# Performance work log

Hardware: AMD Instinct MI355X
Metric: run time of the kernel (lower is better)

## Reference

```python
import jax, jax.numpy as jnp
import numpy as np

B, T, E = 4, 2048, 1024
H = 16
HS = E // H  # head_size = d_model // num_heads, d_model == E here
D_FF = 4 * E
EPS = 1e-5


def _layernorm(x, g, b):
    mu = jnp.mean(x, axis=-1, keepdims=True)
    var = jnp.var(x, axis=-1, keepdims=True)
    return (x - mu) * jax.lax.rsqrt(var + EPS) * g + b


def setup_inputs() -> dict:
    key = jax.random.key(0)
    ks = jax.random.split(key, 12)
    s_e = 1.0 / np.sqrt(E)
    s_ff = 1.0 / np.sqrt(D_FF)
    return {
        "x": jax.random.normal(ks[0], (B, T, E), jnp.float32),
        "ln1_g": jnp.ones((E,), jnp.float32),
        "ln1_b": jnp.zeros((E,), jnp.float32),
        "Wq": jax.random.normal(ks[1], (E, E), jnp.float32) * s_e,
        "bq": jnp.zeros((E,), jnp.float32),
        "Wk": jax.random.normal(ks[2], (E, E), jnp.float32) * s_e,
        "bk": jnp.zeros((E,), jnp.float32),
        "Wv": jax.random.normal(ks[3], (E, E), jnp.float32) * s_e,
        "bv": jnp.zeros((E,), jnp.float32),
        "Wp": jax.random.normal(ks[4], (E, E), jnp.float32) * s_e,
        "bp": jnp.zeros((E,), jnp.float32),
        "ln2_g": jnp.ones((E,), jnp.float32),
        "ln2_b": jnp.zeros((E,), jnp.float32),
        "W1": jax.random.normal(ks[5], (E, D_FF), jnp.float32) * s_e,
        "b1": jnp.zeros((D_FF,), jnp.float32),
        "W2": jax.random.normal(ks[6], (D_FF, E), jnp.float32) * s_ff,
        "b2": jnp.zeros((E,), jnp.float32),
    }


def reference(x, ln1_g, ln1_b, Wq, bq, Wk, bk, Wv, bv, Wp, bp,
              ln2_g, ln2_b, W1, b1, W2, b2):
    # --- attention sublayer ---
    h = _layernorm(x, ln1_g, ln1_b)                      # [B,T,E]
    q = (h @ Wq + bq).reshape(B, T, H, HS)
    k = (h @ Wk + bk).reshape(B, T, H, HS)
    v = (h @ Wv + bv).reshape(B, T, H, HS)
    scores = jnp.einsum('bqhd,bkhd->bhqk', q, k) * (HS ** -0.5)  # [B,H,T,T]
    causal = jnp.tril(jnp.ones((T, T), bool))
    scores = jnp.where(causal, scores, -jnp.inf)
    w = jax.nn.softmax(scores, axis=-1)
    attn = jnp.einsum('bhqk,bkhd->bqhd', w, v).reshape(B, T, H * HS)
    x = x + attn @ Wp + bp
    # --- FFN sublayer ---
    h2 = _layernorm(x, ln2_g, ln2_b)
    x = x + jax.nn.relu(h2 @ W1 + b1) @ W2 + b2
    return x
```

## Files before the change

### kernel.cpp

```cpp
#include <hip/hip_runtime.h>
#include <hip/hip_bf16.h>

#define B_ 4
#define T_ 2048
#define E_ 1024
#define H_ 16
#define HS_ 64
#define DFF_ 4096
#define M_ (B_ * T_)
#define LDQ_ (3 * E_)

typedef __bf16 bf16_t;
typedef __bf16 bf16x4 __attribute__((ext_vector_type(4)));
typedef __bf16 bf16x8 __attribute__((ext_vector_type(8)));
typedef float f32x4 __attribute__((ext_vector_type(4)));

#define AS1 __attribute__((address_space(1)))
#define AS3 __attribute__((address_space(3)))

__device__ __forceinline__ void gload_lds16(const void* g, void* l) {
  __builtin_amdgcn_global_load_lds((AS1 void*)(g), (AS3 void*)(l), 16, 0, 0);
}

__global__ __launch_bounds__(256) void wtrans_kernel(
    const float* __restrict__ W, bf16_t* __restrict__ Wt, int Krows, int Ncols) {
  __shared__ float tile[32][33];
  int tx = threadIdx.x, ty = threadIdx.y;
  int n0 = blockIdx.x * 32, k0 = blockIdx.y * 32;
#pragma unroll
  for (int i = 0; i < 32; i += 8)
    tile[ty + i][tx] = W[(long)(k0 + ty + i) * Ncols + n0 + tx];
  __syncthreads();
#pragma unroll
  for (int i = 0; i < 32; i += 8)
    Wt[(long)(n0 + ty + i) * Krows + k0 + tx] = (bf16_t)tile[tx][ty + i];
}

__global__ __launch_bounds__(256) void bcat_kernel(const float* a, const float* b,
                                                   const float* c, float* o) {
  int i = blockIdx.x * 256 + threadIdx.x;
  o[i] = i < 1024 ? a[i] : (i < 2048 ? b[i - 1024] : c[i - 2048]);
}

__global__ __launch_bounds__(256) void layernorm_kernel(
    const float* __restrict__ in, const float* __restrict__ g,
    const float* __restrict__ b, bf16_t* __restrict__ out) {
  int row = blockIdx.x;
  int tid = threadIdx.x;
  const float4* inr = (const float4*)(in + (long)row * E_);
  float4 v = inr[tid];
  float s = v.x + v.y + v.z + v.w;
  float ss = v.x * v.x + v.y * v.y + v.z * v.z + v.w * v.w;
#pragma unroll
  for (int o = 32; o; o >>= 1) {
    s += __shfl_xor(s, o);
    ss += __shfl_xor(ss, o);
  }
  __shared__ float red[8];
  int wv = tid >> 6;
  if ((tid & 63) == 0) {
    red[wv] = s;
    red[4 + wv] = ss;
  }
  __syncthreads();
  s = red[0] + red[1] + red[2] + red[3];
  ss = red[4] + red[5] + red[6] + red[7];
  float mu = s * (1.f / E_);
  float var = ss * (1.f / E_) - mu * mu;
  float rs = rsqrtf(var + 1e-5f);
  int ci = tid * 4;
  float4 gv = *(const float4*)(g + ci);
  float4 bv = *(const float4*)(b + ci);
  long o0 = (long)row * E_ + ci;
  out[o0 + 0] = (bf16_t)((v.x - mu) * rs * gv.x + bv.x);
  out[o0 + 1] = (bf16_t)((v.y - mu) * rs * gv.y + bv.y);
  out[o0 + 2] = (bf16_t)((v.z - mu) * rs * gv.z + bv.z);
  out[o0 + 3] = (bf16_t)((v.w - mu) * rs * gv.w + bv.w);
}

template <int MODE>
__global__ __launch_bounds__(256) void gemm_bt_kernel(
    const bf16_t* __restrict__ A, const bf16_t* __restrict__ Bt,
    const float* __restrict__ bias, const float* __restrict__ resid,
    void* __restrict__ out, int N, int K) {
  __shared__ bf16_t As[128 * 64];
  __shared__ bf16_t Bs[128 * 64];
  const int tid = threadIdx.x;
  const int lane = tid & 63;
  const int wave = tid >> 6;
  const int wr = wave >> 1, wc = wave & 1;
  const int quad = lane >> 4, l16 = lane & 15;
  const long rowBase = (long)blockIdx.y * 128;
  const long colBase = (long)blockIdx.x * 128;

  f32x4 acc[4][4] = {};

  for (int k0 = 0; k0 < K; k0 += 64) {
#pragma unroll
    for (int i = 0; i < 4; ++i) {
      int c = i * 256 + tid;
      int row = c >> 3;
      int gcol = ((c & 7) ^ (row & 7)) * 8;
      gload_lds16(&A[(rowBase + row) * K + k0 + gcol],
                  As + (i * 256 + wave * 64) * 8);
      gload_lds16(&Bt[(colBase + row) * K + k0 + gcol],
                  Bs + (i * 256 + wave * 64) * 8);
    }
    __syncthreads();
#pragma unroll
    for (int kk = 0; kk < 2; ++kk) {
      bf16x8 af[4], bfr[4];
#pragma unroll
      for (int i = 0; i < 4; ++i) {
        int rowA = wr * 64 + i * 16 + l16;
        af[i] = *(const bf16x8*)&As[(rowA * 8 + ((quad + 4 * kk) ^ (rowA & 7))) * 8];
        int rowB = wc * 64 + i * 16 + l16;
        bfr[i] = *(const bf16x8*)&Bs[(rowB * 8 + ((quad + 4 * kk) ^ (rowB & 7))) * 8];
      }
#pragma unroll
      for (int mi = 0; mi < 4; ++mi)
#pragma unroll
        for (int ni = 0; ni < 4; ++ni)
          acc[mi][ni] = __builtin_amdgcn_mfma_f32_16x16x32_bf16(
              af[mi], bfr[ni], acc[mi][ni], 0, 0, 0);
    }
    __syncthreads();
  }

#pragma unroll
  for (int mi = 0; mi < 4; ++mi) {
#pragma unroll
    for (int ni = 0; ni < 4; ++ni) {
      int colg = (int)colBase + wc * 64 + ni * 16 + l16;
      float bv = bias[colg];
#pragma unroll
      for (int r = 0; r < 4; ++r) {
        long rowg = rowBase + wr * 64 + mi * 16 + quad * 4 + r;
        float v = acc[mi][ni][r] + bv;
        long idx = rowg * N + colg;
        if (MODE == 0) {
          ((bf16_t*)out)[idx] = (bf16_t)v;
        } else if (MODE == 1) {
          ((float*)out)[idx] = v + resid[idx];
        } else {
          ((bf16_t*)out)[idx] = (bf16_t)fmaxf(v, 0.f);
        }
      }
    }
  }
}

__global__ __launch_bounds__(256) void vtrans_kernel(
    const bf16_t* __restrict__ qkv, bf16_t* __restrict__ vt) {
  __shared__ bf16_t tile[32][33];
  int tx = threadIdx.x, ty = threadIdx.y;
  int t0 = blockIdx.x * 32;
  int d0 = (blockIdx.y & 1) * 32;
  int bh = blockIdx.y >> 1;
  int b = bh >> 4, hh = bh & 15;
#pragma unroll
  for (int i = 0; i < 32; i += 8)
    tile[ty + i][tx] =
        qkv[(long)(b * T_ + t0 + ty + i) * LDQ_ + 2 * E_ + hh * HS_ + d0 + tx];
  __syncthreads();
#pragma unroll
  for (int i = 0; i < 32; i += 8)
    vt[((long)bh * HS_ + d0 + ty + i) * T_ + t0 + tx] = tile[tx][ty + i];
}

__global__ __launch_bounds__(256) void flash_attn_kernel(
    const bf16_t* __restrict__ qkv, const bf16_t* __restrict__ vt,
    bf16_t* __restrict__ attn, bf16_t* __restrict__ Opart,
    float* __restrict__ mlpart) {
  int gx = blockIdx.x;
  int ti = 0, sp = 0;
  for (int t = 0; t < 16; ++t) {
    int ns = t / 6 + 1;
    if (gx < ns) { ti = t; sp = gx; break; }
    gx -= ns;
  }
  const int nsplit = ti / 6 + 1;
  const int totIt = 2 * (ti + 1);
  const int jbeg = 12 * sp;
  const int jend = min(jbeg + 12, totIt);

  const int tid = threadIdx.x;
  const int lane = tid & 63, wave = tid >> 6;
  const int quad = lane >> 4, l16 = lane & 15;
  const int bh = blockIdx.y, b = bh >> 4, hh = bh & 15;
  const int q0 = ti * 128;
  const int qw = q0 + wave * 32;

  __shared__ bf16_t Ks[64][72];
  __shared__ bf16_t Vs[64][72];
  __shared__ bf16_t Ps[4][16][72];
  __shared__ float Lrow[4][32];

  const bf16_t* qb = qkv;
  const bf16_t* kb = qkv + E_;

  bf16x8 aq[2][2];
#pragma unroll
  for (int s = 0; s < 2; ++s) {
    long base = (long)(b * T_ + qw + s * 16 + l16) * LDQ_ + hh * HS_ + quad * 8;
    aq[s][0] = *(const bf16x8*)&qb[base];
    aq[s][1] = *(const bf16x8*)&qb[base + 32];
  }

  f32x4 o[2][4] = {};
  float lsum[2][4] = {};

  const int srow = tid >> 3;
  const int scol = (tid & 7) * 8;

  for (int j = jbeg; j < jend; ++j) {
    int kv0 = j * 64;
#pragma unroll
    for (int p = 0; p < 2; ++p) {
      int row = p * 32 + srow;
      *(uint4*)&Ks[row][scol] =
          *(const uint4*)&kb[(long)(b * T_ + kv0 + row) * LDQ_ + hh * HS_ + scol];
      *(uint4*)&Vs[row][scol] =
          *(const uint4*)&vt[((long)bh * HS_ + row) * T_ + kv0 + scol];
    }
    __syncthreads();

#pragma unroll
    for (int s = 0; s < 2; ++s) {
      int qs = qw + s * 16;
      if (kv0 <= qs + 15) {
        f32x4 sc[4];
#pragma unroll
        for (int sub = 0; sub < 4; ++sub) {
          f32x4 t = {};
          t = __builtin_amdgcn_mfma_f32_16x16x32_bf16(
              aq[s][0], *(const bf16x8*)&Ks[sub * 16 + l16][quad * 8], t, 0, 0, 0);
          t = __builtin_amdgcn_mfma_f32_16x16x32_bf16(
              aq[s][1], *(const bf16x8*)&Ks[sub * 16 + l16][32 + quad * 8], t, 0, 0, 0);
          sc[sub] = t * 0.125f;
        }
        if (kv0 + 63 > qs) {
#pragma unroll
          for (int sub = 0; sub < 4; ++sub)
#pragma unroll
            for (int r = 0; r < 4; ++r) {
              int rowq = qs + quad * 4 + r;
              int col = kv0 + sub * 16 + l16;
              if (col > rowq) sc[sub][r] = -INFINITY;
            }
        }
#pragma unroll
        for (int sub = 0; sub < 4; ++sub)
#pragma unroll
          for (int r = 0; r < 4; ++r) sc[sub][r] = __expf(sc[sub][r]);
#pragma unroll
        for (int r = 0; r < 4; ++r)
          lsum[s][r] += (sc[0][r] + sc[1][r]) + (sc[2][r] + sc[3][r]);
#pragma unroll
        for (int sub = 0; sub < 4; ++sub)
#pragma unroll
          for (int r = 0; r < 4; ++r)
            Ps[wave][quad * 4 + r][sub * 16 + l16] = (bf16_t)sc[sub][r];
        bf16x8 ap0 = *(const bf16x8*)&Ps[wave][l16][quad * 8];
        bf16x8 ap1 = *(const bf16x8*)&Ps[wave][l16][32 + quad * 8];
#pragma unroll
        for (int nt = 0; nt < 4; ++nt) {
          o[s][nt] = __builtin_amdgcn_mfma_f32_16x16x32_bf16(
              *(const bf16x8*)&Vs[nt * 16 + l16][quad * 8], ap0, o[s][nt], 0, 0, 0);
          o[s][nt] = __builtin_amdgcn_mfma_f32_16x16x32_bf16(
              *(const bf16x8*)&Vs[nt * 16 + l16][32 + quad * 8], ap1, o[s][nt], 0, 0, 0);
        }
      }
    }
    __syncthreads();
  }

#pragma unroll
  for (int s = 0; s < 2; ++s)
#pragma unroll
    for (int r = 0; r < 4; ++r) {
      float v = lsum[s][r];
#pragma unroll
      for (int off = 1; off <= 8; off <<= 1) v += __shfl_xor(v, off);
      lsum[s][r] = v;
    }
  if (l16 == 0) {
#pragma unroll
    for (int s = 0; s < 2; ++s)
#pragma unroll
      for (int r = 0; r < 4; ++r)
        Lrow[wave][s * 16 + quad * 4 + r] = lsum[s][r];
  }
  float lval[2];
#pragma unroll
  for (int s = 0; s < 2; ++s) lval[s] = Lrow[wave][s * 16 + l16];

  if (nsplit == 1) {
#pragma unroll
    for (int s = 0; s < 2; ++s) {
      float inv = 1.f / lval[s];
      long rowg = (long)b * T_ + qw + s * 16 + l16;
#pragma unroll
      for (int nt = 0; nt < 4; ++nt) {
        bf16x4 pk;
#pragma unroll
        for (int r = 0; r < 4; ++r) pk[r] = (bf16_t)(o[s][nt][r] * inv);
        *(bf16x4*)&attn[rowg * E_ + hh * HS_ + nt * 16 + quad * 4] = pk;
      }
    }
  } else {
    int idx = (ti < 12) ? (ti - 6) * 2 + sp : 12 + (ti - 12) * 3 + sp;
    long slot = (long)bh * 24 + idx;
    bf16_t* op = Opart + slot * (128 * 64);
    float* ml = mlpart + slot * 256;
#pragma unroll
    for (int s = 0; s < 2; ++s) {
      float inv = 1.f / lval[s];
      int rloc = wave * 32 + s * 16 + l16;
#pragma unroll
      for (int nt = 0; nt < 4; ++nt) {
        bf16x4 pk;
#pragma unroll
        for (int r = 0; r < 4; ++r) pk[r] = (bf16_t)(o[s][nt][r] * inv);
        *(bf16x4*)&op[rloc * 64 + nt * 16 + quad * 4] = pk;
      }
      if (quad == 0) ml[rloc] = lval[s];
    }
  }
}

__global__ __launch_bounds__(256) void flash_merge_kernel(
    const bf16_t* __restrict__ Opart, const float* __restrict__ mlpart,
    bf16_t* __restrict__ attn) {
  int ti = 6 + blockIdx.x;
  int bh = blockIdx.y, b = bh >> 4, hh = bh & 15;
  int ns = ti / 6 + 1;
  int base_idx = (ti < 12) ? (ti - 6) * 2 : 12 + (ti - 12) * 3;
  int r = threadIdx.x >> 1;
  int dh = (threadIdx.x & 1) * 32;

  float w[3], den = 0.f;
  for (int s = 0; s < ns; ++s) {
    long slot = (long)bh * 24 + base_idx + s;
    w[s] = mlpart[slot * 256 + r];
    den += w[s];
  }
  float inv = 1.f / den;
  float acc[32];
#pragma unroll
  for (int d = 0; d < 32; ++d) acc[d] = 0.f;
  for (int s = 0; s < ns; ++s) {
    long slot = (long)bh * 24 + base_idx + s;
    const bf16_t* op = Opart + slot * (128 * 64) + r * 64 + dh;
#pragma unroll
    for (int d = 0; d < 32; ++d) acc[d] += w[s] * (float)op[d];
  }
  long rowg = (long)b * T_ + ti * 128 + r;
  bf16_t* dst = attn + rowg * E_ + hh * HS_ + dh;
#pragma unroll
  for (int d = 0; d < 32; ++d) dst[d] = (bf16_t)(acc[d] * inv);
}

extern "C" void kernel_launch(void* const* d_in, const int* in_sizes, int n_in,
                              void* d_out, int out_size, void* d_ws,
                              size_t ws_size, hipStream_t stream) {
  const float* x = (const float*)d_in[0];
  const float* ln1_g = (const float*)d_in[1];
  const float* ln1_b = (const float*)d_in[2];
  const float* Wq = (const float*)d_in[3];
  const float* bq = (const float*)d_in[4];
  const float* Wk = (const float*)d_in[5];
  const float* bk = (const float*)d_in[6];
  const float* Wv = (const float*)d_in[7];
  const float* bv = (const float*)d_in[8];
  const float* Wp = (const float*)d_in[9];
  const float* bp = (const float*)d_in[10];
  const float* ln2_g = (const float*)d_in[11];
  const float* ln2_b = (const float*)d_in[12];
  const float* W1 = (const float*)d_in[13];
  const float* b1 = (const float*)d_in[14];
  const float* W2 = (const float*)d_in[15];
  const float* b2 = (const float*)d_in[16];
  float* out = (float*)d_out;

  const size_t MB = 1ull << 20;
  char* ws = (char*)d_ws;
  bf16_t* wqkvt = (bf16_t*)(ws + 0 * MB);
  bf16_t* wpt   = (bf16_t*)(ws + 6 * MB);
  bf16_t* w1t   = (bf16_t*)(ws + 8 * MB);
  bf16_t* w2t   = (bf16_t*)(ws + 16 * MB);
  float*  bqkv  = (float*)(ws + 24 * MB);
  bf16_t* h     = (bf16_t*)(ws + 25 * MB);
  bf16_t* qkvb  = (bf16_t*)(ws + 41 * MB);
  bf16_t* vt    = (bf16_t*)(ws + 89 * MB);
  float*  xmid  = (float*)(ws + 105 * MB);
  bf16_t* Opart = (bf16_t*)(ws + 105 * MB);
  float* mlpart = (float*)(ws + 131 * MB);
  bf16_t* attn  = h;
  bf16_t* h2    = h;
  bf16_t* ff1   = qkvb;

  dim3 tb(32, 8);
  wtrans_kernel<<<dim3(E_ / 32, E_ / 32), tb, 0, stream>>>(Wq, wqkvt, E_, E_);
  wtrans_kernel<<<dim3(E_ / 32, E_ / 32), tb, 0, stream>>>(Wk, wqkvt + (long)E_ * E_, E_, E_);
  wtrans_kernel<<<dim3(E_ / 32, E_ / 32), tb, 0, stream>>>(Wv, wqkvt + 2l * E_ * E_, E_, E_);
  wtrans_kernel<<<dim3(E_ / 32, E_ / 32), tb, 0, stream>>>(Wp, wpt, E_, E_);
  wtrans_kernel<<<dim3(DFF_ / 32, E_ / 32), tb, 0, stream>>>(W1, w1t, E_, DFF_);
  wtrans_kernel<<<dim3(E_ / 32, DFF_ / 32), tb, 0, stream>>>(W2, w2t, DFF_, E_);
  bcat_kernel<<<12, 256, 0, stream>>>(bq, bk, bv, bqkv);

  layernorm_kernel<<<M_, 256, 0, stream>>>(x, ln1_g, ln1_b, h);

  gemm_bt_kernel<0><<<dim3(3 * E_ / 128, M_ / 128), 256, 0, stream>>>(
      h, wqkvt, bqkv, nullptr, qkvb, 3 * E_, E_);

  vtrans_kernel<<<dim3(T_ / 32, 2 * B_ * H_), tb, 0, stream>>>(qkvb, vt);

  flash_attn_kernel<<<dim3(30, B_ * H_), 256, 0, stream>>>(qkvb, vt, attn,
                                                           Opart, mlpart);
  flash_merge_kernel<<<dim3(10, B_ * H_), 256, 0, stream>>>(Opart, mlpart, attn);

  gemm_bt_kernel<1><<<dim3(E_ / 128, M_ / 128), 256, 0, stream>>>(
      attn, wpt, bp, x, xmid, E_, E_);

  layernorm_kernel<<<M_, 256, 0, stream>>>(xmid, ln2_g, ln2_b, h2);

  gemm_bt_kernel<2><<<dim3(DFF_ / 128, M_ / 128), 256, 0, stream>>>(
      h2, w1t, b1, nullptr, ff1, DFF_, E_);
  gemm_bt_kernel<1><<<dim3(E_ / 128, M_ / 128), 256, 0, stream>>>(
      ff1, w2t, b2, xmid, out, E_, DFF_);
}
```

Baseline: 539.2 us.

## Swap MFMA operand order for row-contiguous outputs and vectorized epilogues

The MFMA A/B operands are swapped in the GEMM and in the attention QK^T, so each lane now holds four consecutive columns of one row instead of one column of four rows. The GEMM epilogue can then use float4 bias/residual loads and 4-wide packed stores instead of scalar strided stores. In attention, the P tile is written to LDS as packed bf16x4, the row-sum reduction shrinks to two cross-quad shuffles with no LDS round trip, and the 1/8 score scale is folded into Q once at load. Folding the scale into bf16 Q is exact because it is a power of two; the main risk is that the causal mask and output indexing must match the transposed accumulator layout.

New measurement: 564.0 us. 4.6% more time.

```diff
diff --git a/kernel.cpp b/kernel.cpp
--- a/kernel.cpp
+++ b/kernel.cpp
@@ -122,29 +122,35 @@
 #pragma unroll
         for (int ni = 0; ni < 4; ++ni)
           acc[mi][ni] = __builtin_amdgcn_mfma_f32_16x16x32_bf16(
-              af[mi], bfr[ni], acc[mi][ni], 0, 0, 0);
+              bfr[ni], af[mi], acc[mi][ni], 0, 0, 0);
     }
     __syncthreads();
   }
 
 #pragma unroll
-  for (int mi = 0; mi < 4; ++mi) {
-#pragma unroll
-    for (int ni = 0; ni < 4; ++ni) {
-      int colg = (int)colBase + wc * 64 + ni * 16 + l16;
-      float bv = bias[colg];
-#pragma unroll
-      for (int r = 0; r < 4; ++r) {
-        long rowg = rowBase + wr * 64 + mi * 16 + quad * 4 + r;
-        float v = acc[mi][ni][r] + bv;
-        long idx = rowg * N + colg;
-        if (MODE == 0) {
-          ((bf16_t*)out)[idx] = (bf16_t)v;
-        } else if (MODE == 1) {
-          ((float*)out)[idx] = v + resid[idx];
-        } else {
-          ((bf16_t*)out)[idx] = (bf16_t)fmaxf(v, 0.f);
-        }
+  for (int ni = 0; ni < 4; ++ni) {
+    int colg = (int)colBase + wc * 64 + ni * 16 + quad * 4;
+    float4 bv4 = *(const float4*)&bias[colg];
+#pragma unroll
+    for (int mi = 0; mi < 4; ++mi) {
+      long rowg = rowBase + wr * 64 + mi * 16 + l16;
+      long idx = rowg * N + colg;
+      f32x4 v = acc[mi][ni];
+      v[0] += bv4.x; v[1] += bv4.y; v[2] += bv4.z; v[3] += bv4.w;
+      if (MODE == 1) {
+        const float4 r4 = *(const float4*)&resid[idx];
+        float4 o4 = make_float4(v[0] + r4.x, v[1] + r4.y, v[2] + r4.z, v[3] + r4.w);
+        *(float4*)&((float*)out)[idx] = o4;
+      } else if (MODE == 0) {
+        bf16x4 pk;
+#pragma unroll
+        for (int r = 0; r < 4; ++r) pk[r] = (bf16_t)v[r];
+        *(bf16x4*)&((bf16_t*)out)[idx] = pk;
+      } else {
+        bf16x4 pk;
+#pragma unroll
+        for (int r = 0; r < 4; ++r) pk[r] = (bf16_t)fmaxf(v[r], 0.f);
+        *(bf16x4*)&((bf16_t*)out)[idx] = pk;
       }
     }
   }
@@ -191,10 +197,9 @@
   const int q0 = ti * 128;
   const int qw = q0 + wave * 32;
 
-  __shared__ bf16_t Ks[64][72];
-  __shared__ bf16_t Vs[64][72];
-  __shared__ bf16_t Ps[4][16][72];
-  __shared__ float Lrow[4][32];
+  __shared__ __align__(16) bf16_t Ks[64][72];
+  __shared__ __align__(16) bf16_t Vs[64][72];
+  __shared__ __align__(16) bf16_t Ps[4][16][72];
 
   const bf16_t* qb = qkv;
   const bf16_t* kb = qkv + E_;
@@ -205,10 +210,15 @@
     long base = (long)(b * T_ + qw + s * 16 + l16) * LDQ_ + hh * HS_ + quad * 8;
     aq[s][0] = *(const bf16x8*)&qb[base];
     aq[s][1] = *(const bf16x8*)&qb[base + 32];
+#pragma unroll
+    for (int e = 0; e < 8; ++e) {
+      aq[s][0][e] = (bf16_t)((float)aq[s][0][e] * 0.125f);
+      aq[s][1][e] = (bf16_t)((float)aq[s][1][e] * 0.125f);
+    }
   }
 
   f32x4 o[2][4] = {};
-  float lsum[2][4] = {};
+  float lsum[2] = {};
 
   const int srow = tid >> 3;
   const int scol = (tid & 7) * 8;
@@ -234,33 +244,36 @@
         for (int sub = 0; sub < 4; ++sub) {
           f32x4 t = {};
           t = __builtin_amdgcn_mfma_f32_16x16x32_bf16(
-              aq[s][0], *(const bf16x8*)&Ks[sub * 16 + l16][quad * 8], t, 0, 0, 0);
+              *(const bf16x8*)&Ks[sub * 16 + l16][quad * 8], aq[s][0], t, 0, 0, 0);
           t = __builtin_amdgcn_mfma_f32_16x16x32_bf16(
-              aq[s][1], *(const bf16x8*)&Ks[sub * 16 + l16][32 + quad * 8], t, 0, 0, 0);
-          sc[sub] = t * 0.125f;
+              *(const bf16x8*)&Ks[sub * 16 + l16][32 + quad * 8], aq[s][1], t, 0, 0, 0);
+          sc[sub] = t;
         }
         if (kv0 + 63 > qs) {
+          int qcol = qs + l16;
 #pragma unroll
           for (int sub = 0; sub < 4; ++sub)
 #pragma unroll
             for (int r = 0; r < 4; ++r) {
-              int rowq = qs + quad * 4 + r;
-              int col = kv0 + sub * 16 + l16;
-              if (col > rowq) sc[sub][r] = -INFINITY;
+              int kvrow = kv0 + sub * 16 + quad * 4 + r;
+              if (kvrow > qcol) sc[sub][r] = -INFINITY;
             }
         }
-#pragma unroll
-        for (int sub = 0; sub < 4; ++sub)
+        float part = 0.f;
+#pragma unroll
+        for (int sub = 0; sub < 4; ++sub) {
 #pragma unroll
           for (int r = 0; r < 4; ++r) sc[sub][r] = __expf(sc[sub][r]);
-#pragma unroll
-        for (int r = 0; r < 4; ++r)
-          lsum[s][r] += (sc[0][r] + sc[1][r]) + (sc[2][r] + sc[3][r]);
-#pragma unroll
-        for (int sub = 0; sub < 4; ++sub)
-#pragma unroll
-          for (int r = 0; r < 4; ++r)
-            Ps[wave][quad * 4 + r][sub * 16 + l16] = (bf16_t)sc[sub][r];
+          part += (sc[sub][0] + sc[sub][1]) + (sc[sub][2] + sc[sub][3]);
+        }
+        lsum[s] += part;
+#pragma unroll
+        for (int sub = 0; sub < 4; ++sub) {
+          bf16x4 pk;
+#pragma unroll
+          for (int r = 0; r < 4; ++r) pk[r] = (bf16_t)sc[sub][r];
+          *(bf16x4*)&Ps[wave][l16][sub * 16 + quad * 4] = pk;
+        }
         bf16x8 ap0 = *(const bf16x8*)&Ps[wave][l16][quad * 8];
         bf16x8 ap1 = *(const bf16x8*)&Ps[wave][l16][32 + quad * 8];
 #pragma unroll
@@ -275,25 +288,14 @@
     __syncthreads();
   }
 
-#pragma unroll
-  for (int s = 0; s < 2; ++s)
-#pragma unroll
-    for (int r = 0; r < 4; ++r) {
-      float v = lsum[s][r];
-#pragma unroll
-      for (int off = 1; off <= 8; off <<= 1) v += __shfl_xor(v, off);
-      lsum[s][r] = v;
-    }
-  if (l16 == 0) {
-#pragma unroll
-    for (int s = 0; s < 2; ++s)
-#pragma unroll
-      for (int r = 0; r < 4; ++r)
-        Lrow[wave][s * 16 + quad * 4 + r] = lsum[s][r];
-  }
   float lval[2];
 #pragma unroll
-  for (int s = 0; s < 2; ++s) lval[s] = Lrow[wave][s * 16 + l16];
+  for (int s = 0; s < 2; ++s) {
+    float v = lsum[s];
+    v += __shfl_xor(v, 16);
+    v += __shfl_xor(v, 32);
+    lval[s] = v;
+  }
 
   if (nsplit == 1) {
 #pragma unroll
```
